# Kernel tuning notes

Hardware: AMD Instinct MI355X
Metric: run time of the kernel (lower is better)

Reference implementation:

```python
import jax, jax.numpy as jnp
import numpy as np

DIM = 512
HEADS = 4
HEAD_DIM = DIM // HEADS
SCALE = HEAD_DIM ** -0.5


def _lin(x, W, b):
    # torch nn.Linear: y = x @ W.T + b, W is [out, in]
    return jnp.einsum('...i,oi->...o', x, W) + b


def setup_inputs() -> dict:
    key = jax.random.key(0)
    ks = jax.random.split(key, 20)
    f1 = jax.random.normal(ks[0], (4, 5, DIM, 10, 10), dtype=jnp.float32)
    f2 = jax.random.normal(ks[1], (4, 75, DIM, 10, 10), dtype=jnp.float32)
    names = ['k1', 'v1', 'q2', 'k2', 'v2', 'o1', 'o2']
    inp = {'f1': f1, 'f2': f2}
    for i, nm in enumerate(names):
        inp['W' + nm] = 0.02 * jax.random.normal(ks[2 + 2 * i], (DIM, DIM), dtype=jnp.float32)
        inp['b' + nm] = 0.02 * jax.random.normal(ks[3 + 2 * i], (DIM,), dtype=jnp.float32)
    return inp


def _forward(f1, f2, Wk1, bk1, Wv1, bv1, Wq2, bq2, Wk2, bk2, Wv2, bv2, Wo1, bo1, Wo2, bo2):
    B, n1, C, H, W = f1.shape
    n2 = f2.shape[1]
    L = H * W
    # [B,n,C,H,W] -> [B,n,L,C]
    f1t = f1.reshape(B, n1, C, L).transpose(0, 1, 3, 2)
    f2t = f2.reshape(B, n2, C, L).transpose(0, 1, 3, 2)

    def split_heads(x, n):  # [B,n,L,C] -> [B,heads,n*L,hd]
        return x.reshape(B, n * L, HEADS, HEAD_DIM).transpose(0, 2, 1, 3)

    def merge_heads(x, n):  # [B,heads,n*L,hd] -> [B,n,L,C]
        return x.transpose(0, 2, 1, 3).reshape(B, n, L, C)

    K1 = split_heads(_lin(f1t, Wk1, bk1), n1)
    V1 = split_heads(_lin(f1t, Wv1, bv1), n1)
    Q2 = split_heads(_lin(f2t, Wq2, bq2), n2)
    K2 = split_heads(_lin(f2t, Wk2, bk2), n2)  # computed as in original, unused downstream
    V2 = split_heads(_lin(f2t, Wv2, bv2), n2)

    # Query attends to support: [B,h,n2*L,n1*L]
    att_q = jax.nn.softmax(jnp.einsum('bhqd,bhkd->bhqk', Q2, K1) * SCALE, axis=-1)
    out2 = jnp.einsum('bhqk,bhkd->bhqd', att_q, V1)
    out2 = _lin(merge_heads(out2, n2), Wo2, bo2)
    out2 = out2.transpose(0, 1, 3, 2).reshape(B, n2, C, H, W)

    # Support attends to query: [B,h,n1*L,n2*L]
    att_s = jax.nn.softmax(jnp.einsum('bhsd,bhqd->bhsq', K1, Q2) * SCALE, axis=-1)
    out1 = jnp.einsum('bhsq,bhqd->bhsd', att_s, V2)
    out1 = _lin(merge_heads(out1, n1), Wo1, bo1)
    out1 = out1.transpose(0, 1, 3, 2).reshape(B, n1, C, H, W)
    return (out1, out2)


def reference(f1, f2, Wk1, bk1, Wv1, bv1, Wq2, bq2, Wk2, bk2, Wv2, bv2, Wo1, bo1, Wo2, bo2):
    return _forward(f1, f2, Wk1, bk1, Wv1, bv1, Wq2, bq2, Wk2, bk2, Wv2, bv2, Wo1, bo1, Wo2, bo2)
```

## Files before the change

kernel.cpp:

```cpp
#include <hip/hip_runtime.h>
#include <hip/hip_bf16.h>


#define QSCL  (0.08838834764831845f * 1.4426950408889634f)
#define KSPL  8
#define NRB2  59
#define NRB1  4

using bf16x8 = __attribute__((ext_vector_type(8))) short;
using f32x4  = __attribute__((ext_vector_type(4))) float;

__device__ inline ushort f2bf(float x) {
    union { float f; unsigned u; } v; v.f = x;
    unsigned r = v.u + 0x7fff + ((v.u >> 16) & 1);
    return (ushort)(r >> 16);
}

__device__ inline void gll16(const ushort* g, ushort* l) {
    __builtin_amdgcn_global_load_lds(
        (const __attribute__((address_space(1))) void*)g,
        (__attribute__((address_space(3))) void*)l, 16, 0, 0);
}

struct PreArgs { const float* w[6]; float s[6]; const float* f1; const float* f2; };

__global__ __launch_bounds__(256) void pre_kernel(
    PreArgs pa, ushort* __restrict__ Wb,
    ushort* __restrict__ f1t, ushort* __restrict__ f2t)
{
    __shared__ ushort Ts[100 * 136];
    const int t   = threadIdx.x;
    const int bid = blockIdx.x;

    if (bid < 1536) {
        const int wsel = bid >> 8;
        const float* src = pa.w[wsel];
        const float sc = pa.s[wsel];
        ushort* d = Wb + (size_t)wsel * 262144;
        const int idx = ((bid & 255) * 256 + t) * 4;
        const float4 v = *(const float4*)(src + idx);
        ushort4 o;
        o.x = f2bf(v.x * sc); o.y = f2bf(v.y * sc);
        o.z = f2bf(v.z * sc); o.w = f2bf(v.w * sc);
        *(ushort4*)(d + idx) = o;
        return;
    }

    const int bn = bid - 1536;
    const float* Xb;
    ushort* Yb;
    if (bn < 20) { Xb = pa.f1 + (size_t)bn * 51200;        Yb = f1t + (size_t)bn * 51200; }
    else         { Xb = pa.f2 + (size_t)(bn - 20) * 51200; Yb = f2t + (size_t)(bn - 20) * 51200; }

    for (int c0 = 0; c0 < 512; c0 += 128) {
        __syncthreads();
        #pragma unroll
        for (int i = 0; i < 50; ++i) {
            const int id = i * 256 + t;
            const int c = id / 100, l = id - c * 100;
            Ts[l * 136 + c] = f2bf(Xb[(size_t)(c0 + c) * 100 + l]);
        }
        __syncthreads();
        #pragma unroll
        for (int i = 0; i < 7; ++i) {
            const int id = i * 256 + t;
            if (id < 1600) {
                const int cg = id & 15, l = id >> 4;
                *(uint4*)(Yb + (size_t)l * 512 + c0 + cg * 8) =
                    *(const uint4*)&Ts[l * 136 + cg * 8];
            }
        }
    }
}

struct GemmJob {
    const ushort* A; const ushort* B;
    const float* bias; void* C;
    size_t sA, sB, sC;
    float bscale;
    int ldC, Mrows, Ncols, gx, gy, fastn, baxis, nblk;
};

struct GemmJobs { GemmJob j0, j1, j2, j3; int ntot; };

template<int EPI>
__global__ __launch_bounds__(256) void gemm_nt(GemmJobs J)
{
    __shared__ ushort smem[17408];
    ushort* As = smem;
    ushort* Bs = smem + 8192;

    const int ntot = J.ntot;
    const int q8 = ntot >> 3, r8 = ntot & 7;
    const int xcd = blockIdx.x & 7, ii = blockIdx.x >> 3;
    const int work = (xcd < r8 ? xcd * (q8 + 1)
                               : r8 * (q8 + 1) + (xcd - r8) * q8) + ii;

    GemmJob j; int id;
    {
        const int c0 = J.j0.nblk;
        const int c1 = c0 + J.j1.nblk;
        const int c2 = c1 + J.j2.nblk;
        if (work < c0)      { j = J.j0; id = work; }
        else if (work < c1) { j = J.j1; id = work - c0; }
        else if (work < c2) { j = J.j2; id = work - c1; }
        else                { j = J.j3; id = work - c2; }
    }

    const int fx = id % j.gx;
    const int rem = id / j.gx;
    const int fy = rem % j.gy;
    const int bz = rem / j.gy;
    const int m0 = (j.fastn ? fy : fx) * 128;
    const int n0 = (j.fastn ? fx : fy) * 128;

    const int t    = threadIdx.x;
    const int lane = t & 63;
    const int w    = t >> 6;
    const int mw   = (w >> 1) * 64;
    const int nw   = (w & 1) * 64;
    const int Mrows = j.Mrows, Ncols = j.Ncols, ldC = j.ldC;
    const ushort* Ab = j.A + (size_t)bz * j.sA;
    const ushort* Bb = j.B + (size_t)bz * j.sB;
    const float* bias = j.bias;

    f32x4 acc[4][4];
    #pragma unroll
    for (int i = 0; i < 4; ++i)
        #pragma unroll
        for (int jj = 0; jj < 4; ++jj) acc[i][jj] = (f32x4){0.f, 0.f, 0.f, 0.f};

    const int lr = lane >> 3;
    const int cb = lane & 7;

    for (int k0 = 0; k0 < 512; k0 += 64) {
        if (k0) __syncthreads();
        #pragma unroll
        for (int i = 0; i < 4; ++i) {
            const int row = w * 32 + i * 8 + lr;
            const int ar = min(m0 + row, Mrows - 1);
            gll16(Ab + (size_t)ar * 512 + k0 + ((cb ^ (row & 7)) * 8),
                  As + (w * 32 + i * 8) * 64);
            const int br = min(n0 + row, Ncols - 1);
            gll16(Bb + (size_t)br * 512 + k0 + ((cb ^ (row & 7)) * 8),
                  Bs + (w * 32 + i * 8) * 64);
        }
        __syncthreads();
        #pragma unroll
        for (int ks = 0; ks < 2; ++ks) {
            bf16x8 af[4], bv[4];
            #pragma unroll
            for (int mf = 0; mf < 4; ++mf) {
                const int row = mw + mf * 16 + (lane & 15);
                af[mf] = *(const bf16x8*)((const char*)As + row * 128 +
                          ((ks * 64 + (lane >> 4) * 16) ^ ((row & 7) << 4)));
            }
            #pragma unroll
            for (int nf = 0; nf < 4; ++nf) {
                const int row = nw + nf * 16 + (lane & 15);
                bv[nf] = *(const bf16x8*)((const char*)Bs + row * 128 +
                          ((ks * 64 + (lane >> 4) * 16) ^ ((row & 7) << 4)));
            }
            #pragma unroll
            for (int mf = 0; mf < 4; ++mf)
                #pragma unroll
                for (int nf = 0; nf < 4; ++nf)
                    acc[mf][nf] = __builtin_amdgcn_mfma_f32_16x16x32_bf16(
                        af[mf], bv[nf], acc[mf][nf], 0, 0, 0);
        }
    }
    __syncthreads();

    if (EPI == 0) {
        float bcol[4];
        if (j.baxis == 1) {
            #pragma unroll
            for (int nf = 0; nf < 4; ++nf)
                bcol[nf] = bias[n0 + nw + nf * 16 + (lane & 15)] * j.bscale;
        }
        ushort* Ts = smem;
        #pragma unroll
        for (int mf = 0; mf < 4; ++mf) {
            #pragma unroll
            for (int r = 0; r < 4; ++r) {
                const int row = mw + mf * 16 + (lane >> 4) * 4 + r;
                const float brow = (j.baxis == 0) ? bias[m0 + row] * j.bscale : 0.f;
                #pragma unroll
                for (int nf = 0; nf < 4; ++nf) {
                    const int col = nw + nf * 16 + (lane & 15);
                    const float v = acc[mf][nf][r] +
                                    ((j.baxis == 1) ? bcol[nf] : brow);
                    Ts[row * 136 + col] = f2bf(v);
                }
            }
        }
        __syncthreads();
        ushort* Cb = (ushort*)j.C + (size_t)bz * j.sC;
        #pragma unroll
        for (int i = 0; i < 8; ++i) {
            const int id2 = i * 256 + t;
            const int row = id2 >> 4, cg = id2 & 15;
            if (m0 + row < Mrows)
                *(uint4*)(Cb + (size_t)(m0 + row) * ldC + n0 + cg * 8) =
                    *(const uint4*)&Ts[row * 136 + cg * 8];
        }
    } else {
        float* Ts2 = (float*)smem;
        float* Cb = (float*)j.C + (size_t)bz * j.sC;
        const int colL = t & 127;
        const int rb2 = t >> 7;
        const int tg = n0 + colL;
        int nIdx = 0, lIdx = 0;
        if (tg < Ncols) { nIdx = tg / 100; lIdx = tg - nIdx * 100; }
        #pragma unroll
        for (int h = 0; h < 2; ++h) {
            __syncthreads();
            if ((mw >> 6) == h) {
                #pragma unroll
                for (int mf = 0; mf < 4; ++mf) {
                    #pragma unroll
                    for (int r = 0; r < 4; ++r) {
                        const int rowl = mf * 16 + (lane >> 4) * 4 + r;
                        const float brow = bias[m0 + h * 64 + rowl];
                        #pragma unroll
                        for (int nf = 0; nf < 4; ++nf) {
                            const int col = nw + nf * 16 + (lane & 15);
                            Ts2[rowl * 132 + col] = acc[mf][nf][r] + brow;
                        }
                    }
                }
            }
            __syncthreads();
            if (tg < Ncols) {
                float* dst = Cb + (size_t)nIdx * 51200 + lIdx;
                #pragma unroll
                for (int i = 0; i < 32; ++i) {
                    const int rowl = i * 2 + rb2;
                    const int c = m0 + h * 64 + rowl;
                    dst[(size_t)c * 100] = Ts2[rowl * 132 + colL];
                }
            }
        }
    }
}

__global__ __launch_bounds__(256, 2) void attn_mfma_kernel(
    const ushort* __restrict__ Q2, const ushort* __restrict__ K1,
    const ushort* __restrict__ V1t, const ushort* __restrict__ V2t,
    ushort* __restrict__ A2, float* __restrict__ PartO, float* __restrict__ Pml)
{
    __shared__ ushort Ks[2 * 64 * 128];
    __shared__ ushort Vs[2 * 128 * 64];

    const int t    = threadIdx.x;
    const int lane = t & 63;
    const int w    = t >> 6;

    const int flat = blockIdx.x;
    const int xcd = flat & 7, ii = flat >> 3;
    const bool dir2 = (ii >= 64);
    int rb, h, b, sp = 0;
    if (dir2) {
        const int w2 = xcd * 118 + (ii - 64);
        rb = w2 % NRB2;
        const int hb = w2 / NRB2;
        h = hb & 3; b = hb >> 2;
    } else {
        const int w1 = xcd * 64 + ii;
        rb = w1 & 3; sp = (w1 >> 2) & 7;
        const int hb = w1 >> 5;
        h = hb & 3; b = hb >> 2;
    }

    const int TR = dir2 ? 7500 : 500;
    const int TK = dir2 ? 500 : 7500;
    const int strideV = dir2 ? 512 : 7552;
    const ushort* R  = dir2 ? Q2 : K1;
    const ushort* Kt = dir2 ? K1 : Q2;
    const ushort* Vt = dir2 ? V1t : V2t;

    const int r0 = rb * 128;
    const int ho = h * 128;

    int kbeg = 0, kend = TK;
    if (!dir2) {
        kbeg = sp * 938;
        kend = kbeg + 938; if (kend > TK) kend = TK;
    }

    bf16x8 qa0[4], qa1[4];
    {
        const ushort* Rb = R + (size_t)b * TR * 512;
        const int q0 = min(r0 + w * 32 + (lane & 15), TR - 1);
        const int q1 = min(r0 + w * 32 + 16 + (lane & 15), TR - 1);
        const ushort* qp0 = Rb + (size_t)q0 * 512 + ho + (lane >> 4) * 8;
        const ushort* qp1 = Rb + (size_t)q1 * 512 + ho + (lane >> 4) * 8;
        #pragma unroll
        for (int s = 0; s < 4; ++s) {
            qa0[s] = *(const bf16x8*)(qp0 + s * 32);
            qa1[s] = *(const bf16x8*)(qp1 + s * 32);
        }
    }

    const ushort* Kb = Kt + (size_t)b * TK * 512;
    const ushort* Vb = Vt + ((size_t)b * 512 + ho) * strideV;

    const int krow_i = lane >> 4;
    const int kcol   = (lane & 15) * 8;
    const int vrow_i = lane >> 3;
    const int vcol   = (lane & 7) * 8;
    const int gq     = lane >> 4;

    float m_run0 = -3.0e38f, l_run0 = 0.f;
    float m_run1 = -3.0e38f, l_run1 = 0.f;
    f32x4 acc0[8], acc1[8];
    #pragma unroll
    for (int g = 0; g < 8; ++g) {
        acc0[g] = (f32x4){0.f, 0.f, 0.f, 0.f};
        acc1[g] = (f32x4){0.f, 0.f, 0.f, 0.f};
    }

    #pragma unroll
    for (int i = 0; i < 4; ++i) {
        const int kr = w * 16 + i * 4 + krow_i;
        gll16(Kb + (size_t)(kbeg + kr) * 512 + ho + (kcol ^ ((kr & 7) << 3)),
              Ks + (w * 16 + i * 4) * 128);
        const int vd = w * 32 + i * 8 + vrow_i;
        gll16(Vb + (size_t)vd * strideV + kbeg + (vcol ^ ((vd & 7) << 3)),
              Vs + (w * 32 + i * 8) * 64);
    }
    asm volatile("s_waitcnt vmcnt(0)" ::: "memory");
    __builtin_amdgcn_s_barrier();
    __builtin_amdgcn_sched_barrier(0);

    int c = 0;
    for (int kbase = kbeg; kbase < kend; kbase += 64, ++c) {
        const ushort* KsC = Ks + (c & 1) * 8192;
        const ushort* VsC = Vs + (c & 1) * 8192;
        ushort* KsN = Ks + ((c + 1) & 1) * 8192;
        ushort* VsN = Vs + ((c + 1) & 1) * 8192;

        const int kn = kbase + 64;
        if (kn < kend) {
            #pragma unroll
            for (int i = 0; i < 4; ++i) {
                const int kr = w * 16 + i * 4 + krow_i;
                gll16(Kb + (size_t)(kn + kr) * 512 + ho + (kcol ^ ((kr & 7) << 3)),
                      KsN + (w * 16 + i * 4) * 128);
                const int vd = w * 32 + i * 8 + vrow_i;
                gll16(Vb + (size_t)vd * strideV + kn + (vcol ^ ((vd & 7) << 3)),
                      VsN + (w * 32 + i * 8) * 64);
            }
        }

        f32x4 sf0[4], sf1[4];
        __builtin_amdgcn_s_setprio(1);
        #pragma unroll
        for (int f = 0; f < 4; ++f) {
            f32x4 s0 = (f32x4){0.f, 0.f, 0.f, 0.f};
            f32x4 s1 = (f32x4){0.f, 0.f, 0.f, 0.f};
            const int kr = f * 16 + (lane & 15);
            const int kb2 = kr * 256, sw = (kr & 7) << 4, g16 = gq * 16;
            #pragma unroll
            for (int s4 = 0; s4 < 4; ++s4) {
                bf16x8 kf = *(const bf16x8*)((const char*)KsC + kb2 + ((s4 * 64 + g16) ^ sw));
                s0 = __builtin_amdgcn_mfma_f32_16x16x32_bf16(kf, qa0[s4], s0, 0, 0, 0);
                s1 = __builtin_amdgcn_mfma_f32_16x16x32_bf16(kf, qa1[s4], s1, 0, 0, 0);
            }
            sf0[f] = s0; sf1[f] = s1;
        }
        __builtin_amdgcn_s_setprio(0);

        if (kbase + 64 > kend) {
            #pragma unroll
            for (int f = 0; f < 4; ++f)
                #pragma unroll
                for (int r = 0; r < 4; ++r)
                    if (kbase + f * 16 + gq * 4 + r >= kend) {
                        sf0[f][r] = -3.0e38f; sf1[f][r] = -3.0e38f;
                    }
        }
        {
            float mx = sf0[0][0];
            #pragma unroll
            for (int f = 0; f < 4; ++f)
                #pragma unroll
                for (int r = 0; r < 4; ++r) mx = fmaxf(mx, sf0[f][r]);
            mx = fmaxf(mx, __shfl_xor(mx, 16));
            mx = fmaxf(mx, __shfl_xor(mx, 32));
            if (__any(mx > m_run0 + 11.0f)) {
                const float mn = fmaxf(m_run0, mx);
                const float sc = __builtin_amdgcn_exp2f(m_run0 - mn);
                m_run0 = mn; l_run0 *= sc;
                float scal4[4];
                #pragma unroll
                for (int r = 0; r < 4; ++r)
                    scal4[r] = __shfl(sc, (lane & 48) + gq * 4 + r);
                #pragma unroll
                for (int g = 0; g < 8; ++g)
                    #pragma unroll
                    for (int r = 0; r < 4; ++r) acc0[g][r] *= scal4[r];
            }
            float rs = 0.f;
            #pragma unroll
            for (int f = 0; f < 4; ++f)
                #pragma unroll
                for (int r = 0; r < 4; ++r) {
                    const float p = __builtin_amdgcn_exp2f(sf0[f][r] - m_run0);
                    sf0[f][r] = p; rs += p;
                }
            rs += __shfl_xor(rs, 16);
            rs += __shfl_xor(rs, 32);
            l_run0 += rs;
        }
        {
            float mx = sf1[0][0];
            #pragma unroll
            for (int f = 0; f < 4; ++f)
                #pragma unroll
                for (int r = 0; r < 4; ++r) mx = fmaxf(mx, sf1[f][r]);
            mx = fmaxf(mx, __shfl_xor(mx, 16));
            mx = fmaxf(mx, __shfl_xor(mx, 32));
            if (__any(mx > m_run1 + 11.0f)) {
                const float mn = fmaxf(m_run1, mx);
                const float sc = __builtin_amdgcn_exp2f(m_run1 - mn);
                m_run1 = mn; l_run1 *= sc;
                float scal4[4];
                #pragma unroll
                for (int r = 0; r < 4; ++r)
                    scal4[r] = __shfl(sc, (lane & 48) + gq * 4 + r);
                #pragma unroll
                for (int g = 0; g < 8; ++g)
                    #pragma unroll
                    for (int r = 0; r < 4; ++r) acc1[g][r] *= scal4[r];
            }
            float rs = 0.f;
            #pragma unroll
            for (int f = 0; f < 4; ++f)
                #pragma unroll
                for (int r = 0; r < 4; ++r) {
                    const float p = __builtin_amdgcn_exp2f(sf1[f][r] - m_run1);
                    sf1[f][r] = p; rs += p;
                }
            rs += __shfl_xor(rs, 16);
            rs += __shfl_xor(rs, 32);
            l_run1 += rs;
        }

        union { uint u[4]; bf16x8 v; } pa00, pa01, pa10, pa11;
        {
            uint pk0[4][2], pk1[4][2];
            #pragma unroll
            for (int f = 0; f < 4; ++f) {
                asm("v_cvt_pk_bf16_f32 %0, %1, %2" : "=v"(pk0[f][0]) : "v"(sf0[f][0]), "v"(sf0[f][1]));
                asm("v_cvt_pk_bf16_f32 %0, %1, %2" : "=v"(pk0[f][1]) : "v"(sf0[f][2]), "v"(sf0[f][3]));
                asm("v_cvt_pk_bf16_f32 %0, %1, %2" : "=v"(pk1[f][0]) : "v"(sf1[f][0]), "v"(sf1[f][1]));
                asm("v_cvt_pk_bf16_f32 %0, %1, %2" : "=v"(pk1[f][1]) : "v"(sf1[f][2]), "v"(sf1[f][3]));
            }
            #pragma unroll
            for (int u = 0; u < 4; ++u) {
                const int srcl = (lane & 15) + ((lane & 16) << 1) + ((u >> 1) << 4);
                const uint a0 = (uint)__shfl((int)pk0[0][u & 1], srcl);
                const uint b0 = (uint)__shfl((int)pk0[1][u & 1], srcl);
                const uint a1 = (uint)__shfl((int)pk0[2][u & 1], srcl);
                const uint b1 = (uint)__shfl((int)pk0[3][u & 1], srcl);
                pa00.u[u] = (lane & 32) ? b0 : a0;
                pa01.u[u] = (lane & 32) ? b1 : a1;
                const uint c0 = (uint)__shfl((int)pk1[0][u & 1], srcl);
                const uint d0 = (uint)__shfl((int)pk1[1][u & 1], srcl);
                const uint c1 = (uint)__shfl((int)pk1[2][u & 1], srcl);
                const uint d1 = (uint)__shfl((int)pk1[3][u & 1], srcl);
                pa10.u[u] = (lane & 32) ? d0 : c0;
                pa11.u[u] = (lane & 32) ? d1 : c1;
            }
        }

        {
            const int g16 = gq * 16;
            __builtin_amdgcn_s_setprio(1);
            #pragma unroll
            for (int g = 0; g < 8; ++g) {
                const int dr = g * 16 + (lane & 15);
                const int vb = dr * 128, vsw = (dr & 7) << 4;
                bf16x8 v0 = *(const bf16x8*)((const char*)VsC + vb + ((g16) ^ vsw));
                bf16x8 v1 = *(const bf16x8*)((const char*)VsC + vb + ((64 + g16) ^ vsw));
                acc0[g] = __builtin_amdgcn_mfma_f32_16x16x32_bf16(pa00.v, v0, acc0[g], 0, 0, 0);
                acc0[g] = __builtin_amdgcn_mfma_f32_16x16x32_bf16(pa01.v, v1, acc0[g], 0, 0, 0);
                acc1[g] = __builtin_amdgcn_mfma_f32_16x16x32_bf16(pa10.v, v0, acc1[g], 0, 0, 0);
                acc1[g] = __builtin_amdgcn_mfma_f32_16x16x32_bf16(pa11.v, v1, acc1[g], 0, 0, 0);
            }
            __builtin_amdgcn_s_setprio(0);
        }

        asm volatile("s_waitcnt vmcnt(0)" ::: "memory");
        __builtin_amdgcn_s_barrier();
        __builtin_amdgcn_sched_barrier(0);
    }

    if (dir2) {
        float linv0[4], linv1[4];
        #pragma unroll
        for (int r = 0; r < 4; ++r) {
            linv0[r] = 1.f / __shfl(l_run0, (lane & 48) + gq * 4 + r);
            linv1[r] = 1.f / __shfl(l_run1, (lane & 48) + gq * 4 + r);
        }
        char* Ts = (char*)Ks;
        #pragma unroll
        for (int r = 0; r < 4; ++r) {
            const int rl0 = w * 32 + (gq << 2) + r;
            const int rl1 = rl0 + 16;
            const int sw0 = (rl0 & 7) << 4, sw1 = (rl1 & 7) << 4;
            #pragma unroll
            for (int g = 0; g < 8; ++g) {
                const int cb2 = g * 32 + (lane & 15) * 2;
                *(ushort*)(Ts + rl0 * 256 + (cb2 ^ sw0)) = f2bf(acc0[g][r] * linv0[r]);
                *(ushort*)(Ts + rl1 * 256 + (cb2 ^ sw1)) = f2bf(acc1[g][r] * linv1[r]);
            }
        }
        __syncthreads();
        #pragma unroll
        for (int i = 0; i < 8; ++i) {
            const int id = i * 256 + t;
            const int row = id >> 4, cg = id & 15;
            const int grow = r0 + row;
            if (grow < TR)
                *(uint4*)(A2 + ((size_t)b * TR + grow) * 512 + ho + cg * 8) =
                    *(const uint4*)(Ts + row * 256 + ((cg * 16) ^ ((row & 7) << 4)));
        }
    } else {
        const size_t tile = (((size_t)b * 4 + h) * NRB1 + rb) * KSPL + sp;
        float* Po = PartO + tile * (128 * 128);
        float* Pm = Pml + tile * 256;
        #pragma unroll
        for (int r = 0; r < 4; ++r) {
            const int row0 = w * 32 + (gq << 2) + r;
            float* pp0 = Po + row0 * 128 + (lane & 15);
            #pragma unroll
            for (int g = 0; g < 8; ++g) pp0[g * 16] = acc0[g][r];
            const int row1 = w * 32 + 16 + (gq << 2) + r;
            float* pp1 = Po + row1 * 128 + (lane & 15);
            #pragma unroll
            for (int g = 0; g < 8; ++g) pp1[g * 16] = acc1[g][r];
        }
        if (lane < 16) {
            Pm[w * 32 + lane] = m_run0;
            Pm[w * 32 + 16 + lane] = m_run1;
            Pm[128 + w * 32 + lane] = l_run0;
            Pm[128 + w * 32 + 16 + lane] = l_run1;
        }
    }
}

__global__ __launch_bounds__(256) void attn_combine_kernel(
    const float* __restrict__ PartO, const float* __restrict__ Pml,
    ushort* __restrict__ Aout, int TR)
{
    const int t = threadIdx.x;
    const int rb = blockIdx.x >> 1, half = blockIdx.x & 1;
    const int h = blockIdx.y, b = blockIdx.z;
    const int row = half * 64 + (t >> 2);
    const int dq = (t & 3) * 32;
    const int r0 = rb * 128;
    const size_t tbase = (((size_t)b * 4 + h) * NRB1 + rb) * KSPL;

    float M = -3.0e38f;
    #pragma unroll
    for (int i = 0; i < KSPL; ++i)
        M = fmaxf(M, Pml[(tbase + i) * 256 + row]);
    float wt[KSPL], L = 0.f;
    #pragma unroll
    for (int i = 0; i < KSPL; ++i) {
        const float wi = __builtin_amdgcn_exp2f(Pml[(tbase + i) * 256 + row] - M);
        wt[i] = wi;
        L += wi * Pml[(tbase + i) * 256 + 128 + row];
    }
    if (r0 + row >= TR) return;
    const float invL = 1.f / L;

    float o[32];
    #pragma unroll
    for (int j = 0; j < 32; ++j) o[j] = 0.f;
    #pragma unroll
    for (int i = 0; i < KSPL; ++i) {
        const float* pp = PartO + (tbase + i) * (128 * 128) + row * 128 + dq;
        #pragma unroll
        for (int j = 0; j < 32; j += 4) {
            const float4 v = *(const float4*)(pp + j);
            o[j] += wt[i] * v.x; o[j+1] += wt[i] * v.y;
            o[j+2] += wt[i] * v.z; o[j+3] += wt[i] * v.w;
        }
    }
    ushort* Ab = Aout + ((size_t)b * TR + r0 + row) * 512 + h * 128 + dq;
    #pragma unroll
    for (int j = 0; j < 32; j += 4) {
        ushort4 v;
        v.x = f2bf(o[j] * invL); v.y = f2bf(o[j+1] * invL);
        v.z = f2bf(o[j+2] * invL); v.w = f2bf(o[j+3] * invL);
        *(ushort4*)(Ab + j) = v;
    }
}

extern "C" void kernel_launch(void* const* d_in, const int* in_sizes, int n_in,
                              void* d_out, int out_size, void* d_ws, size_t ws_size,
                              hipStream_t stream) {
    const float* f1  = (const float*)d_in[0];
    const float* f2  = (const float*)d_in[1];
    const float* Wk1 = (const float*)d_in[2];
    const float* bk1 = (const float*)d_in[3];
    const float* Wv1 = (const float*)d_in[4];
    const float* bv1 = (const float*)d_in[5];
    const float* Wq2 = (const float*)d_in[6];
    const float* bq2 = (const float*)d_in[7];
    const float* Wv2 = (const float*)d_in[10];
    const float* bv2 = (const float*)d_in[11];
    const float* Wo1 = (const float*)d_in[12];
    const float* bo1 = (const float*)d_in[13];
    const float* Wo2 = (const float*)d_in[14];
    const float* bo2 = (const float*)d_in[15];
    float* out = (float*)d_out;

    ushort* f1t = (ushort*)d_ws;
    ushort* f2t = f1t + (size_t)1024000;
    ushort* Wb  = f2t + (size_t)15360000;
    ushort* K1  = Wb  + (size_t)1572864;
    ushort* Q2  = K1  + (size_t)1024000;
    ushort* V1t = Q2  + (size_t)15360000;
    ushort* V2t = V1t + (size_t)1048576;
    ushort* A1  = V2t + (size_t)15466496;
    ushort* A2  = A1  + (size_t)1024000;
    float* PartO = (float*)(A2 + (size_t)15360000);
    float* Pml   = PartO + (size_t)512*128*128;

    const dim3 blk(256);

    const ushort* Wk1b = Wb;
    const ushort* Wv1b = Wb + 262144;
    const ushort* Wq2b = Wb + 2*262144;
    const ushort* Wv2b = Wb + 3*262144;
    const ushort* Wo1b = Wb + 4*262144;
    const ushort* Wo2b = Wb + 5*262144;

    PreArgs pa;
    pa.w[0]=Wk1; pa.w[1]=Wv1; pa.w[2]=Wq2; pa.w[3]=Wv2; pa.w[4]=Wo1; pa.w[5]=Wo2;
    pa.s[0]=1.f; pa.s[1]=1.f; pa.s[2]=QSCL; pa.s[3]=1.f; pa.s[4]=1.f; pa.s[5]=1.f;
    pa.f1 = f1; pa.f2 = f2;
    pre_kernel<<<dim3(1856), blk, 0, stream>>>(pa, Wb, f1t, f2t);

    GemmJob jK {f1t, Wk1b, bk1, K1, 0, 0, 0, 1.f, 512, 2000, 512,
                4, 16, 1, 1, 64};
    GemmJob jQ {f2t, Wq2b, bq2, Q2, 0, 0, 0, QSCL, 512, 30000, 512,
                4, 235, 1, 1, 940};
    GemmJob jV1{Wv1b, f1t, bv1, V1t, 0, (size_t)500*512, (size_t)512*512, 1.f,
                512, 512, 500, 4, 4, 0, 0, 64};
    GemmJob jV2{Wv2b, f2t, bv2, V2t, 0, (size_t)7500*512, (size_t)512*7552, 1.f,
                7552, 512, 7500, 4, 59, 0, 0, 944};
    GemmJobs JP{jK, jQ, jV1, jV2, 2012};
    gemm_nt<0><<<dim3(2012), blk, 0, stream>>>(JP);

    attn_mfma_kernel<<<dim3(1456), dim3(256), 0, stream>>>(
        Q2, K1, V1t, V2t, A2, PartO, Pml);
    attn_combine_kernel<<<dim3(8, 4, 4), blk, 0, stream>>>(PartO, Pml, A1, 500);

    GemmJob jO1{Wo1b, A1, bo1, out, 0, (size_t)500*512, (size_t)5*51200, 1.f,
                0, 512, 500, 4, 4, 0, 0, 64};
    GemmJob jO2{Wo2b, A2, bo2, out + (size_t)1024000, 0, (size_t)7500*512,
                (size_t)75*51200, 1.f, 0, 512, 7500, 4, 59, 0, 0, 944};
    GemmJob jZ{};
    GemmJobs JO{jO1, jO2, jZ, jZ, 1008};
    gemm_nt<2><<<dim3(1008), blk, 0, stream>>>(JO);
}
```

Before: 234.4 us.

## Fuse split-K attention combine into attention kernel via last-arriver atomic counter

Removes the separate attn_combine_kernel launch. Each split-K partial block of the support-direction attention bumps a per-tile atomic counter after writing its partial O and m/l values. The last arriving block then merges all KSPL partials and writes the bf16 A1 rows. The counters are zeroed in pre_kernel. This saves a kernel launch and the gap between launches, at the cost of threadfences, an atomic per block, and serial combine work on 64 blocks.

```diff
diff --git a/kernel.cpp b/kernel.cpp
--- a/kernel.cpp
+++ b/kernel.cpp
@@ -26,13 +26,15 @@
 
 __global__ __launch_bounds__(256) void pre_kernel(
     PreArgs pa, ushort* __restrict__ Wb,
-    ushort* __restrict__ f1t, ushort* __restrict__ f2t)
+    ushort* __restrict__ f1t, ushort* __restrict__ f2t,
+    uint* __restrict__ TileCnt)
 {
     __shared__ ushort Ts[100 * 136];
     const int t   = threadIdx.x;
     const int bid = blockIdx.x;
 
     if (bid < 1536) {
+        if (bid == 0 && t < 64) TileCnt[t] = 0;
         const int wsel = bid >> 8;
         const float* src = pa.w[wsel];
         const float sc = pa.s[wsel];
@@ -247,7 +249,9 @@
 __global__ __launch_bounds__(256, 2) void attn_mfma_kernel(
     const ushort* __restrict__ Q2, const ushort* __restrict__ K1,
     const ushort* __restrict__ V1t, const ushort* __restrict__ V2t,
-    ushort* __restrict__ A2, float* __restrict__ PartO, float* __restrict__ Pml)
+    ushort* __restrict__ A2, ushort* __restrict__ A1,
+    float* __restrict__ PartO, float* __restrict__ Pml,
+    uint* __restrict__ TileCnt)
 {
     __shared__ ushort Ks[2 * 64 * 128];
     __shared__ ushort Vs[2 * 128 * 64];
@@ -528,7 +532,8 @@
                     *(const uint4*)(Ts + row * 256 + ((cg * 16) ^ ((row & 7) << 4)));
         }
     } else {
-        const size_t tile = (((size_t)b * 4 + h) * NRB1 + rb) * KSPL + sp;
+        const int tidx = (b * 4 + h) * NRB1 + rb;
+        const size_t tile = (size_t)tidx * KSPL + sp;
         float* Po = PartO + tile * (128 * 128);
         float* Pm = Pml + tile * 256;
         #pragma unroll
@@ -548,55 +553,59 @@
             Pm[128 + w * 32 + lane] = l_run0;
             Pm[128 + w * 32 + 16 + lane] = l_run1;
         }
-    }
-}
-
-__global__ __launch_bounds__(256) void attn_combine_kernel(
-    const float* __restrict__ PartO, const float* __restrict__ Pml,
-    ushort* __restrict__ Aout, int TR)
-{
-    const int t = threadIdx.x;
-    const int rb = blockIdx.x >> 1, half = blockIdx.x & 1;
-    const int h = blockIdx.y, b = blockIdx.z;
-    const int row = half * 64 + (t >> 2);
-    const int dq = (t & 3) * 32;
-    const int r0 = rb * 128;
-    const size_t tbase = (((size_t)b * 4 + h) * NRB1 + rb) * KSPL;
-
-    float M = -3.0e38f;
-    #pragma unroll
-    for (int i = 0; i < KSPL; ++i)
-        M = fmaxf(M, Pml[(tbase + i) * 256 + row]);
-    float wt[KSPL], L = 0.f;
-    #pragma unroll
-    for (int i = 0; i < KSPL; ++i) {
-        const float wi = __builtin_amdgcn_exp2f(Pml[(tbase + i) * 256 + row] - M);
-        wt[i] = wi;
-        L += wi * Pml[(tbase + i) * 256 + 128 + row];
-    }
-    if (r0 + row >= TR) return;
-    const float invL = 1.f / L;
-
-    float o[32];
-    #pragma unroll
-    for (int j = 0; j < 32; ++j) o[j] = 0.f;
-    #pragma unroll
-    for (int i = 0; i < KSPL; ++i) {
-        const float* pp = PartO + (tbase + i) * (128 * 128) + row * 128 + dq;
-        #pragma unroll
-        for (int j = 0; j < 32; j += 4) {
-            const float4 v = *(const float4*)(pp + j);
-            o[j] += wt[i] * v.x; o[j+1] += wt[i] * v.y;
-            o[j+2] += wt[i] * v.z; o[j+3] += wt[i] * v.w;
-        }
-    }
-    ushort* Ab = Aout + ((size_t)b * TR + r0 + row) * 512 + h * 128 + dq;
-    #pragma unroll
-    for (int j = 0; j < 32; j += 4) {
-        ushort4 v;
-        v.x = f2bf(o[j] * invL); v.y = f2bf(o[j+1] * invL);
-        v.z = f2bf(o[j+2] * invL); v.w = f2bf(o[j+3] * invL);
-        *(ushort4*)(Ab + j) = v;
+
+        __threadfence();
+        if (t == 0) {
+            const uint old = atomicAdd(&TileCnt[tidx], 1u);
+            ((volatile uint*)Vs)[0] = old;
+        }
+        __syncthreads();
+        const uint arriv = ((volatile uint*)Vs)[0];
+        if (arriv == KSPL - 1) {
+            __threadfence();
+            const size_t tb2 = (size_t)tidx * KSPL;
+            #pragma unroll
+            for (int half = 0; half < 2; ++half) {
+                const int row = half * 64 + (t >> 2);
+                const int dq = (t & 3) * 32;
+                float M = -3.0e38f;
+                #pragma unroll
+                for (int i = 0; i < KSPL; ++i)
+                    M = fmaxf(M, Pml[(tb2 + i) * 256 + row]);
+                float wt[KSPL], L = 0.f;
+                #pragma unroll
+                for (int i = 0; i < KSPL; ++i) {
+                    const float wi = __builtin_amdgcn_exp2f(Pml[(tb2 + i) * 256 + row] - M);
+                    wt[i] = wi;
+                    L += wi * Pml[(tb2 + i) * 256 + 128 + row];
+                }
+                const int grow = r0 + row;
+                if (grow < 500) {
+                    const float invL = 1.f / L;
+                    float o[32];
+                    #pragma unroll
+                    for (int jj = 0; jj < 32; ++jj) o[jj] = 0.f;
+                    #pragma unroll
+                    for (int i = 0; i < KSPL; ++i) {
+                        const float* pp = PartO + (tb2 + i) * (128 * 128) + row * 128 + dq;
+                        #pragma unroll
+                        for (int jj = 0; jj < 32; jj += 4) {
+                            const float4 v = *(const float4*)(pp + jj);
+                            o[jj]   += wt[i] * v.x; o[jj+1] += wt[i] * v.y;
+                            o[jj+2] += wt[i] * v.z; o[jj+3] += wt[i] * v.w;
+                        }
+                    }
+                    ushort* Ab = A1 + ((size_t)b * 500 + grow) * 512 + ho + dq;
+                    #pragma unroll
+                    for (int jj = 0; jj < 32; jj += 4) {
+                        ushort4 v;
+                        v.x = f2bf(o[jj] * invL);   v.y = f2bf(o[jj+1] * invL);
+                        v.z = f2bf(o[jj+2] * invL); v.w = f2bf(o[jj+3] * invL);
+                        *(ushort4*)(Ab + jj) = v;
+                    }
+                }
+            }
+        }
     }
 }
 
@@ -630,6 +639,7 @@
     ushort* A2  = A1  + (size_t)1024000;
     float* PartO = (float*)(A2 + (size_t)15360000);
     float* Pml   = PartO + (size_t)512*128*128;
+    uint* TileCnt = (uint*)(Pml + (size_t)512*256);
 
     const dim3 blk(256);
 
@@ -644,7 +654,7 @@
     pa.w[0]=Wk1; pa.w[1]=Wv1; pa.w[2]=Wq2; pa.w[3]=Wv2; pa.w[4]=Wo1; pa.w[5]=Wo2;
     pa.s[0]=1.f; pa.s[1]=1.f; pa.s[2]=QSCL; pa.s[3]=1.f; pa.s[4]=1.f; pa.s[5]=1.f;
     pa.f1 = f1; pa.f2 = f2;
-    pre_kernel<<<dim3(1856), blk, 0, stream>>>(pa, Wb, f1t, f2t);
+    pre_kernel<<<dim3(1856), blk, 0, stream>>>(pa, Wb, f1t, f2t, TileCnt);
 
     GemmJob jK {f1t, Wk1b, bk1, K1, 0, 0, 0, 1.f, 512, 2000, 512,
                 4, 16, 1, 1, 64};
@@ -658,8 +668,7 @@
     gemm_nt<0><<<dim3(2012), blk, 0, stream>>>(JP);
 
     attn_mfma_kernel<<<dim3(1456), dim3(256), 0, stream>>>(
-        Q2, K1, V1t, V2t, A2, PartO, Pml);
-    attn_combine_kernel<<<dim3(8, 4, 4), blk, 0, stream>>>(PartO, Pml, A1, 500);
+        Q2, K1, V1t, V2t, A2, A1, PartO, Pml, TileCnt);
 
     GemmJob jO1{Wo1b, A1, bo1, out, 0, (size_t)500*512, (size_t)5*51200, 1.f,
                 0, 512, 500, 4, 4, 0, 0, 64};
```

After: 303.5 us. 29.5% more time.
